# Kernel optimization log

Measured on AMD Instinct MI355X. Metric: run time of the kernel, lower is better.

## Reference

```python
import jax, jax.numpy as jnp
import numpy as np

B, S, D, H, DFF = 2, 2048, 1024, 16, 4096
DK = D // H
EPS = 1e-05


def setup_inputs() -> dict:
    key = jax.random.key(0)
    ks = jax.random.split(key, 10)
    s = 0.02
    return {
        "x": jax.random.normal(ks[0], (B, S, D), jnp.float32),
        "src_mask": jnp.ones((B, 1, 1, S), jnp.int32),
        "wq": jax.random.normal(ks[1], (D, D), jnp.float32) * s,
        "wk": jax.random.normal(ks[2], (D, D), jnp.float32) * s,
        "wv": jax.random.normal(ks[3], (D, D), jnp.float32) * s,
        "wo": jax.random.normal(ks[4], (D, D), jnp.float32) * s,
        "w1": jax.random.normal(ks[5], (D, DFF), jnp.float32) * s,
        "b1": jnp.zeros((DFF,), jnp.float32),
        "w2": jax.random.normal(ks[6], (DFF, D), jnp.float32) * s,
        "b2": jnp.zeros((D,), jnp.float32),
        "gamma1": jnp.ones((), jnp.float32),
        "beta1": jnp.ones((), jnp.float32),
        "gamma2": jnp.ones((), jnp.float32),
        "beta2": jnp.ones((), jnp.float32),
    }


def layer_norm(x, gamma, beta):
    # torch.var uses unbiased estimator (ddof=1); gamma/beta are scalars
    mean = jnp.mean(x, axis=-1, keepdims=True)
    var = jnp.var(x, axis=-1, keepdims=True, ddof=1)
    return (x - mean) * gamma / jnp.sqrt(var + EPS) + beta


def mha(x, wq, wk, wv, wo):
    # Note: source's masked_fill is non-in-place with discarded result -> mask has no effect.
    q = (x @ wq).reshape(B, S, H, DK).transpose(0, 2, 1, 3)
    k = (x @ wk).reshape(B, S, H, DK).transpose(0, 2, 1, 3)
    v = (x @ wv).reshape(B, S, H, DK).transpose(0, 2, 1, 3)
    scores = jnp.einsum('bhqd,bhkd->bhqk', q, k) / jnp.sqrt(jnp.float32(DK))
    attn = jax.nn.softmax(scores, axis=-1)
    out = jnp.einsum('bhqk,bhkd->bhqd', attn, v)
    out = out.transpose(0, 2, 1, 3).reshape(B, S, D)
    return out @ wo


def reference(x, src_mask, wq, wk, wv, wo, w1, b1, w2, b2,
              gamma1, beta1, gamma2, beta2):
    # residual 1: attention (dropout = identity in eval)
    x = layer_norm(x + mha(x, wq, wk, wv, wo), gamma1, beta1)
    # residual 2: FFN
    ff = jax.nn.relu(x @ w1 + b1) @ w2 + b2
    x = layer_norm(x + ff, gamma2, beta2)
    return x
```

## Files before the change

kernel.cpp:

```cpp
#include <hip/hip_runtime.h>
#include <cstdio>

constexpr int B_   = 2;
constexpr int S_   = 2048;
constexpr int D_   = 1024;
constexpr int H_   = 16;
constexpr int DFF_ = 4096;
constexpr int DK_  = D_ / H_;
constexpr int M_   = B_ * S_;
constexpr float EPS_ = 1e-5f;
constexpr size_t MEGE = 1u << 20;
constexpr size_t QKV_STRIDE = 4 * MEGE;
constexpr float QSCALE_ = 0.18033688011112042f;

typedef __attribute__((ext_vector_type(8))) short bf16x8;
typedef __attribute__((ext_vector_type(4))) float f32x4;

__device__ __forceinline__ float bf2f(unsigned int u) {
    return __uint_as_float(u << 16);
}
__device__ __forceinline__ unsigned short f2bf(float f) {
    unsigned int u = __float_as_uint(f);
    unsigned int r = u + 0x7fffu + ((u >> 16) & 1u);
    return (unsigned short)(r >> 16);
// ... 27 lines not shown
        Wt[(size_t)(n0 + ty + p * 8) * K + k0 + tx] = f2bf(t[tx * 33 + ty + p * 8]);
}

__global__ __launch_bounds__(256)
void prep_k(const float* __restrict__ wq, const float* __restrict__ wk,
            const float* __restrict__ wv, const float* __restrict__ wo,
            const float* __restrict__ w1, const float* __restrict__ w2,
            const float* __restrict__ x,
            unsigned short* __restrict__ wqt, unsigned short* __restrict__ wkt,
            unsigned short* __restrict__ wvt, unsigned short* __restrict__ wot,
            unsigned short* __restrict__ w1t, unsigned short* __restrict__ w2t,
            unsigned short* __restrict__ xb)
{
    __shared__ float t[32 * 33];
    const int bid = blockIdx.x;
    if (bid < 4096) {
        const int z = bid >> 10, rem = bid & 1023;
        const float* W = (z == 0) ? wq : (z == 1) ? wk : (z == 2) ? wv : wo;
        unsigned short* Wt = (z == 0) ? wqt : (z == 1) ? wkt : (z == 2) ? wvt : wot;
        tr32(W, Wt, D_, D_, rem & 31, rem >> 5, t);
    } else if (bid < 8192) {
        const int rem = bid - 4096;
        tr32(w1, w1t, D_, DFF_, rem & 127, rem >> 7, t);
    } else if (bid < 12288) {
        const int rem = bid - 8192;
        tr32(w2, w2t, DFF_, D_, rem & 31, rem >> 5, t);
    } else {
        const int i = (bid - 12288) * 256 + threadIdx.x;
        float4 f = reinterpret_cast<const float4*>(x)[i];
        ushort4 u;
        u.x = f2bf(f.x); u.y = f2bf(f.y); u.z = f2bf(f.z); u.w = f2bf(f.w);
        reinterpret_cast<ushort4*>(xb)[i] = u;
    }
}

template<int OMODE, bool RELU>
__global__ __launch_bounds__(1024, 1)
void mg3_k(const unsigned short* __restrict__ A,
           const unsigned short* __restrict__ Bt,
           const float* __restrict__ bias,
           unsigned short* __restrict__ C,
           int M, int N, int K, int Kld)
{
    __shared__ __align__(16) unsigned short As[2][256 * 64];
    __shared__ __align__(16) unsigned short Bs[2][256 * 64];

    const int tid = threadIdx.x;
    const int w = tid >> 6, lane = tid & 63;
    const int l15 = lane & 15, quad = lane >> 4;
    const int wm = w >> 2, wn = w & 3;
    const int m0 = blockIdx.y * 256, n0 = blockIdx.x * 256;
    const int NT = K >> 6;

    const int srow = lane >> 3;
    const int schk = (lane & 7) ^ srow;
    const int rsw  = l15 & 7;

    f32x4 acc[4][4];
    #pragma unroll
    for (int i = 0; i < 4; ++i)
        #pragma unroll
        for (int j = 0; j < 4; ++j) acc[i][j] = (f32x4){0.f, 0.f, 0.f, 0.f};

    auto stageAB = [&](int tile) {
        if (tile >= NT) return;
        const int buf = tile & 1;
// ... 46 lines not shown
        mm16();
        rd(cur, 1);
        __builtin_amdgcn_s_barrier();
        asm volatile("s_waitcnt lgkmcnt(0)" ::: "memory");
        mm16();
    }

    #pragma unroll
    for (int i = 0; i < 4; ++i)
        #pragma unroll
        for (int r = 0; r < 4; ++r) {
            const int m = m0 + wm * 64 + i * 16 + quad * 4 + r;
            #pragma unroll
            for (int j = 0; j < 4; ++j) {
                const int n = n0 + wn * 64 + j * 16 + l15;
                float v = acc[i][j][r];
                if (bias) v += bias[n];
                if (RELU) v = fmaxf(v, 0.0f);
                size_t o;
                if (OMODE == 2) {
                    int mat = n >> 10, nn = n & 1023;
                    int bb = m >> 11, s = m & 2047;
                    int h = nn >> 6, dk = nn & 63;
                    if (mat == 0) v *= QSCALE_;
                    o = (size_t)mat * QKV_STRIDE + (((size_t)bb * H_ + h) * S_ + s) * DK_ + dk;
                } else {
                    o = (size_t)m * N + n;
                }
                C[o] = f2bf(v);
            }
        }
}

template<int BM, int OMODE, bool RELU>
__global__ __launch_bounds__(512, 2)
void mg2_k(const unsigned short* __restrict__ A,
           const unsigned short* __restrict__ Bt,
           const float* __restrict__ bias,
           unsigned short* __restrict__ C,
           int M, int N, int K, int Kld)
{
    constexpr int MI  = BM / 64;
    constexpr int AMH = (BM == 128) ? 2 : 1;
    __shared__ __align__(16) unsigned short As[2][BM * 64];
    __shared__ __align__(16) unsigned short Bs[2][256 * 64];

    const int z = blockIdx.z;
    A  += (size_t)z * K;
    Bt += (size_t)z * K;
    C  += (size_t)z * ((size_t)M * N);

    const int tid  = threadIdx.x;
    const int w    = tid >> 6, lane = tid & 63;
    const int l15  = lane & 15, quad = lane >> 4;
    const int wm   = w >> 2, wn = w & 3;
    const int m0   = blockIdx.y * BM, n0 = blockIdx.x * 256;
    const int NT   = K >> 6;

    const int srow = lane >> 3;
    const int schk = (lane & 7) ^ srow;
    const int rsw  = l15 & 7;

    f32x4 acc[2][MI][2][2];
    #pragma unroll
    for (int mh = 0; mh < 2; ++mh)
        #pragma unroll
        for (int mi = 0; mi < MI; ++mi)
            #pragma unroll
            for (int nh = 0; nh < 2; ++nh)
                #pragma unroll
                for (int nj = 0; nj < 2; ++nj)
                    acc[mh][mi][nh][nj] = (f32x4){0.f, 0.f, 0.f, 0.f};

    bf16x8 aA[AMH][MI][2];
    bf16x8 b0[2][2], b1[2][2];

    auto stage = [&](int tile, int type) {
        if (tile >= NT) return;
        const int buf = tile & 1;
        unsigned short* dst; const unsigned short* src; int r0;
        if (BM == 256) {
            if      (type == 0) { dst = &As[buf][0];        src = A;  r0 = m0; }
            else if (type == 1) { dst = &Bs[buf][0];        src = Bt; r0 = n0; }
            else if (type == 2) { dst = &Bs[buf][128 * 64]; src = Bt; r0 = n0 + 128; }
            else                { dst = &As[buf][128 * 64]; src = A;  r0 = m0 + 128; }
        } else {
            if      (type == 0) { dst = &Bs[buf][0];        src = Bt; r0 = n0; }
            else if (type == 1) { dst = &As[buf][0];        src = A;  r0 = m0; }
            else                { dst = &Bs[buf][128 * 64]; src = Bt; r0 = n0 + 128; }
        }
        const int k0 = tile * 64;
        #pragma unroll
        for (int g = 0; g < 2; ++g) {
            const int r = w * 16 + g * 8 + srow;
            gload_lds16(src + (size_t)(r0 + r) * Kld + k0 + schk * 8,
                        dst + (w * 16 + g * 8) * 64);
        }
    };
    auto rdA = [&](int buf, int mh, int amh) {
        const unsigned short* base = &As[buf][(BM == 256 && mh) ? 128 * 64 : 0];
        #pragma unroll
        for (int mi = 0; mi < MI; ++mi) {
            const int row = (BM == 256) ? (wm * 64 + mi * 16 + l15)
                                        : (wm * 64 + mh * 32 + mi * 16 + l15);
            const unsigned short* rp = base + row * 64;
            aA[amh][mi][0] = *reinterpret_cast<const bf16x8*>(rp + ((quad    ) ^ rsw) * 8);
            aA[amh][mi][1] = *reinterpret_cast<const bf16x8*>(rp + ((quad + 4) ^ rsw) * 8);
        }
    };
    auto rdB = [&](int buf, int nh, bf16x8 (&b)[2][2]) {
        const unsigned short* base = &Bs[buf][nh ? 128 * 64 : 0];
        #pragma unroll
        for (int nj = 0; nj < 2; ++nj) {
            const int row = wn * 32 + nj * 16 + l15;
            const unsigned short* rp = base + row * 64;
            b[nj][0] = *reinterpret_cast<const bf16x8*>(rp + ((quad    ) ^ rsw) * 8);
            b[nj][1] = *reinterpret_cast<const bf16x8*>(rp + ((quad + 4) ^ rsw) * 8);
        }
    };
    auto mm = [&](int mh, int amh, int nh, bf16x8 (&b)[2][2]) {
        __builtin_amdgcn_s_setprio(1);
        #pragma unroll
        for (int mi = 0; mi < MI; ++mi)
            #pragma unroll
            for (int nj = 0; nj < 2; ++nj) {
                acc[mh][mi][nh][nj] = __builtin_amdgcn_mfma_f32_16x16x32_bf16(
                    aA[amh][mi][0], b[nj][0], acc[mh][mi][nh][nj], 0, 0, 0);
                acc[mh][mi][nh][nj] = __builtin_amdgcn_mfma_f32_16x16x32_bf16(
                    aA[amh][mi][1], b[nj][1], acc[mh][mi][nh][nj], 0, 0, 0);
            }
        __builtin_amdgcn_s_setprio(0);
    };

    if (BM == 256) {
        stage(0, 0); stage(0, 1); stage(0, 2); stage(0, 3);
        stage(1, 0); stage(1, 1); stage(1, 2);
    } else {
        stage(0, 0); stage(0, 1); stage(0, 2);
        stage(1, 0); stage(1, 1);
    }

    for (int t = 0; t < NT; ++t) {
        const int cur = t & 1;
        if (t == NT - 1)    asm volatile("s_waitcnt vmcnt(0)" ::: "memory");
        else if (BM == 256) asm volatile("s_waitcnt vmcnt(6)" ::: "memory");
        else                asm volatile("s_waitcnt vmcnt(4)" ::: "memory");
        __builtin_amdgcn_s_barrier();

        if (BM == 256) {
            rdA(cur, 0, 0); rdB(cur, 0, b0); stage(t + 1, 3);
            __builtin_amdgcn_s_barrier();
            asm volatile("s_waitcnt lgkmcnt(0)" ::: "memory");
            mm(0, 0, 0, b0);
            __builtin_amdgcn_s_barrier();
            rdB(cur, 1, b1); stage(t + 2, 0);
            __builtin_amdgcn_s_barrier();
            asm volatile("s_waitcnt lgkmcnt(0)" ::: "memory");
            mm(0, 0, 1, b1);
            __builtin_amdgcn_s_barrier();
            rdA(cur, 1, 0); stage(t + 2, 1);
            __builtin_amdgcn_s_barrier();
            asm volatile("s_waitcnt lgkmcnt(0)" ::: "memory");
            mm(1, 0, 0, b0);
            __builtin_amdgcn_s_barrier();
            stage(t + 2, 2);
            __builtin_amdgcn_s_barrier();
            asm volatile("s_waitcnt lgkmcnt(0)" ::: "memory");
            mm(1, 0, 1, b1);
        } else {
            rdA(cur, 0, 0); rdA(cur, 1, 1); rdB(cur, 0, b0); stage(t + 1, 2);
            __builtin_amdgcn_s_barrier();
            asm volatile("s_waitcnt lgkmcnt(0)" ::: "memory");
            mm(0, 0, 0, b0); mm(1, 1, 0, b0);
            __builtin_amdgcn_s_barrier();
            rdB(cur, 1, b1); stage(t + 2, 0); stage(t + 2, 1);
            __builtin_amdgcn_s_barrier();
            asm volatile("s_waitcnt lgkmcnt(0)" ::: "memory");
            mm(0, 0, 1, b1); mm(1, 1, 1, b1);
        }
    }

    #pragma unroll
    for (int mh = 0; mh < 2; ++mh)
        #pragma unroll
        for (int mi = 0; mi < MI; ++mi) {
            const int mrow = (BM == 256) ? (mh * 128 + wm * 64 + mi * 16)
                                         : (wm * 64 + mh * 32 + mi * 16);
            #pragma unroll
            for (int r = 0; r < 4; ++r) {
                const int m = m0 + mrow + quad * 4 + r;
                #pragma unroll
                for (int nh = 0; nh < 2; ++nh)
                    #pragma unroll
                    for (int nj = 0; nj < 2; ++nj) {
                        const int n = n0 + nh * 128 + wn * 32 + nj * 16 + l15;
                        float v = acc[mh][mi][nh][nj][r];
                        if (bias) v += bias[n];
                        if (RELU) v = fmaxf(v, 0.0f);
                        size_t o;
                        if (OMODE == 2) {
                            int mat = n >> 10, nn = n & 1023;
                            int b = m >> 11, s = m & 2047;
                            int h = nn >> 6, dk = nn & 63;
                            if (mat == 0) v *= QSCALE_;
                            o = (size_t)mat * QKV_STRIDE + (((size_t)b * H_ + h) * S_ + s) * DK_ + dk;
                        } else {
                            o = (size_t)m * N + n;
                        }
                        C[o] = f2bf(v);
                    }
            }
        }
}

__device__ __forceinline__ float wave_sum(float v) {
    #pragma unroll
    for (int off = 32; off > 0; off >>= 1) v += __shfl_down(v, off, 64);
    return v;
}

constexpr int TQ_ = 128;
constexpr int TK_ = 64;
constexpr int NT_ = S_ / TK_;

__global__ __launch_bounds__(512)
void fattn_k(const unsigned short* __restrict__ Qm, const unsigned short* __restrict__ Km,
             const unsigned short* __restrict__ Vm, unsigned short* __restrict__ O)
{
    const int bh  = blockIdx.x >> 4;
    const int qt  = blockIdx.x & 15;
    const int tid = threadIdx.x;
    const int w = tid >> 6, lane = tid & 63;
    const int quad = lane >> 4, l15 = lane & 15;
    const int sw = l15 & 7;

    __shared__ __align__(16) unsigned short Ks[2][TK_][64];
    __shared__ __align__(16) unsigned short Vt[2][80][64];
    __shared__ __align__(16) unsigned short Ps[8][16][64];

    bf16x8 qf0, qf1;
    {
        const unsigned short* qp = Qm + ((size_t)bh * S_ + qt * TQ_ + w * 16 + l15) * DK_;
        qf0 = *reinterpret_cast<const bf16x8*>(qp + quad * 8);
        qf1 = *reinterpret_cast<const bf16x8*>(qp + 32 + quad * 8);
    }

    f32x4 o[4];
    f32x4 o4;
    #pragma unroll
    for (int n = 0; n < 4; ++n) o[n] = (f32x4){0.f, 0.f, 0.f, 0.f};
    o4 = (f32x4){0.f, 0.f, 0.f, 0.f};

    const unsigned short* kg0 = Km + (size_t)bh * S_ * DK_;
    const unsigned short* vg0 = Vm + (size_t)bh * S_ * DK_;
    const int dgrp = tid >> 4;
    const int vkp  = tid & 15;
    const int srow = lane >> 3;
    const int schk = (lane & 7) ^ srow;

    auto stageK = [&](int t, int buf) {
        const unsigned short* src = kg0 + (size_t)t * TK_ * DK_;
        const int wk = w - 4;
        #pragma unroll
        for (int g = 0; g < 2; ++g) {
            const int r0 = wk * 16 + g * 8;
            gload_lds16(src + (size_t)(r0 + srow) * DK_ + schk * 8, &Ks[buf][r0][0]);
        }
    };
    auto loadV = [&](int t, ushort4 (&vp)[4]) {
        const unsigned short* vg = vg0 + (size_t)t * TK_ * DK_;
        #pragma unroll
        for (int p = 0; p < 4; ++p)
            vp[p] = reinterpret_cast<const ushort4*>(vg + (size_t)(vkp + p * 16) * DK_)[dgrp];
    };
    auto storeVt = [&](int buf, ushort4 (&vp)[4]) {
        char* base = reinterpret_cast<char*>(&Vt[buf][dgrp * 4][0]);
        const int cs = vkp >> 1, ch = (vkp & 1) << 3;
        ushort4 pk;
        pk.x = vp[0].x; pk.y = vp[1].x; pk.z = vp[2].x; pk.w = vp[3].x;
        *reinterpret_cast<ushort4*>(base + 0 * 128 + (((cs ^ ((dgrp * 4 + 0) & 7)) << 4) + ch)) = pk;
        pk.x = vp[0].y; pk.y = vp[1].y; pk.z = vp[2].y; pk.w = vp[3].y;
        *reinterpret_cast<ushort4*>(base + 1 * 128 + (((cs ^ ((dgrp * 4 + 1) & 7)) << 4) + ch)) = pk;
        pk.x = vp[0].z; pk.y = vp[1].z; pk.z = vp[2].z; pk.w = vp[3].z;
        *reinterpret_cast<ushort4*>(base + 2 * 128 + (((cs ^ ((dgrp * 4 + 2) & 7)) << 4) + ch)) = pk;
        pk.x = vp[0].w; pk.y = vp[1].w; pk.z = vp[2].w; pk.w = vp[3].w;
        *reinterpret_cast<ushort4*>(base + 3 * 128 + (((cs ^ ((dgrp * 4 + 3) & 7)) << 4) + ch)) = pk;
    };

    if (w >= 4) stageK(0, 0);
    else {
        ushort4 vp0[4];
        loadV(0, vp0);
        storeVt(0, vp0);
    }
    for (int idx = tid; idx < 2 * 16 * 64; idx += 512) {
        const int b  = idx >> 10;
        const int rr = (idx >> 6) & 15;
        const int cc = idx & 63;
        Vt[b][64 + rr][((cc >> 3) ^ (rr & 7)) * 8 + (cc & 7)] =
            (rr == 0) ? (unsigned short)0x3F80 : (unsigned short)0;
    }

    for (int t = 0; t < NT_; ++t) {
        const int cur = t & 1, nxt = cur ^ 1;
        __syncthreads();

        const bool hn = (t + 1 < NT_);
        ushort4 vp[4];
        if (hn) { if (w >= 4) stageK(t + 1, nxt); else loadV(t + 1, vp); }

        f32x4 s[4];
        __builtin_amdgcn_s_setprio(1);
        #pragma unroll
        for (int n = 0; n < 4; ++n) {
            const unsigned short* kp = &Ks[cur][n * 16 + l15][0];
            bf16x8 b0 = *reinterpret_cast<const bf16x8*>(kp + ((quad ^ sw) << 3));
            bf16x8 b1 = *reinterpret_cast<const bf16x8*>(kp + (((quad + 4) ^ sw) << 3));
            f32x4 a2 = (f32x4){0.f, 0.f, 0.f, 0.f};
            a2 = __builtin_amdgcn_mfma_f32_16x16x32_bf16(qf0, b0, a2, 0, 0, 0);
            a2 = __builtin_amdgcn_mfma_f32_16x16x32_bf16(qf1, b1, a2, 0, 0, 0);
            s[n] = a2;
        }
        __builtin_amdgcn_s_setprio(0);

        #pragma unroll
        for (int r = 0; r < 4; ++r) {
            ushort4 pk;
            pk.x = f2bf_rz(exp2_fast(s[0][r]));
            pk.y = f2bf_rz(exp2_fast(s[1][r]));
            pk.z = f2bf_rz(exp2_fast(s[2][r]));
            pk.w = f2bf_rz(exp2_fast(s[3][r]));
            const int R = quad * 4 + r;
            *reinterpret_cast<ushort4*>(
                reinterpret_cast<char*>(&Ps[w][R][0]) +
                ((((l15 >> 1) ^ (R & 7)) << 4) + ((l15 & 1) << 3))) = pk;
        }

        if (hn && w < 4) storeVt(nxt, vp);

        bf16x8 pa0, pa1;
        {
            const unsigned short* pp = &Ps[w][l15][0];
            pa0 = *reinterpret_cast<const bf16x8*>(pp + ((quad ^ sw) << 3));
            pa1 = *reinterpret_cast<const bf16x8*>(pp + (((quad + 4) ^ sw) << 3));
        }
        __builtin_amdgcn_s_setprio(1);
        #pragma unroll
        for (int n = 0; n < 4; ++n) {
            const unsigned short* vb = &Vt[cur][n * 16 + l15][0];
            bf16x8 vb0 = *reinterpret_cast<const bf16x8*>(vb + ((quad ^ sw) << 3));
            bf16x8 vb1 = *reinterpret_cast<const bf16x8*>(vb + (((quad + 4) ^ sw) << 3));
            o[n] = __builtin_amdgcn_mfma_f32_16x16x32_bf16(pa0, vb0, o[n], 0, 0, 0);
            o[n] = __builtin_amdgcn_mfma_f32_16x16x32_bf16(pa1, vb1, o[n], 0, 0, 0);
        }
        {
            const unsigned short* vb = &Vt[cur][64 + l15][0];
            bf16x8 vb40 = *reinterpret_cast<const bf16x8*>(vb + ((quad ^ sw) << 3));
            bf16x8 vb41 = *reinterpret_cast<const bf16x8*>(vb + (((quad + 4) ^ sw) << 3));
            o4 = __builtin_amdgcn_mfma_f32_16x16x32_bf16(pa0, vb40, o4, 0, 0, 0);
            o4 = __builtin_amdgcn_mfma_f32_16x16x32_bf16(pa1, vb41, o4, 0, 0, 0);
        }
        __builtin_amdgcn_s_setprio(0);
    }

    const int b = bh >> 4, h = bh & 15;
    #pragma unroll
    for (int r = 0; r < 4; ++r) {
        float lrv = __shfl(o4[r], lane & 0x30, 64);
        float inv = 1.0f / lrv;
        int q = qt * TQ_ + w * 16 + quad * 4 + r;
        unsigned short* op = O + ((size_t)b * S_ + q) * D_ + h * DK_;
        #pragma unroll
        for (int n = 0; n < 4; ++n)
            op[n * 16 + l15] = f2bf(o[n][r] * inv);
    }
}

template<bool HAS_BIAS, bool RES_F32, bool OUT_F32>
__global__ __launch_bounds__(256)
void lnr_k(const unsigned short* __restrict__ P0, const unsigned short* __restrict__ P1,
           const void* __restrict__ res, const float* __restrict__ bias,
           const float* __restrict__ gp, const float* __restrict__ bp,
           void* __restrict__ Out)
{
    const int row = blockIdx.x;
    const int tid = threadIdx.x;
    const int lane = tid & 63, wave = tid >> 6;
    __shared__ float rs[4], rss[4];

    const size_t i4 = (size_t)row * 256 + tid;
    const ushort4 a = reinterpret_cast<const ushort4*>(P0)[i4];
    const ushort4 b = reinterpret_cast<const ushort4*>(P1)[i4];
    float v0 = bf2f(a.x) + bf2f(b.x);
    float v1 = bf2f(a.y) + bf2f(b.y);
    float v2 = bf2f(a.z) + bf2f(b.z);
    float v3 = bf2f(a.w) + bf2f(b.w);
    if (RES_F32) {
        float4 rv = reinterpret_cast<const float4*>(res)[i4];
        v0 += rv.x; v1 += rv.y; v2 += rv.z; v3 += rv.w;
    } else {
        ushort4 rv = reinterpret_cast<const ushort4*>(res)[i4];
        v0 += bf2f(rv.x); v1 += bf2f(rv.y); v2 += bf2f(rv.z); v3 += bf2f(rv.w);
    }
    if (HAS_BIAS) {
        float4 bv = reinterpret_cast<const float4*>(bias)[tid];
        v0 += bv.x; v1 += bv.y; v2 += bv.z; v3 += bv.w;
    }

// ... 27 lines not shown
                              void* d_out, int out_size, void* d_ws, size_t ws_size,
                              hipStream_t stream)
{
    const float* x   = (const float*)d_in[0];
    const float* wq  = (const float*)d_in[2];
    const float* wk  = (const float*)d_in[3];
    const float* wv  = (const float*)d_in[4];
    const float* wo  = (const float*)d_in[5];
    const float* w1  = (const float*)d_in[6];
    const float* b1  = (const float*)d_in[7];
    const float* w2  = (const float*)d_in[8];
    const float* b2  = (const float*)d_in[9];
    const float* g1  = (const float*)d_in[10];
    const float* be1 = (const float*)d_in[11];
    const float* g2  = (const float*)d_in[12];
    const float* be2 = (const float*)d_in[13];

    unsigned short* ws = (unsigned short*)d_ws;
    const size_t need_bytes = 32 * MEGE * 2;
    if (ws_size < need_bytes) {
        fprintf(stderr, "kernel_launch: ws too small (%zu < %zu)\n", ws_size, need_bytes);
    }
    unsigned short* wqt = ws + 0 * MEGE;
    unsigned short* wkt = ws + 1 * MEGE;
    unsigned short* wvt = ws + 2 * MEGE;
    unsigned short* wot = ws + 3 * MEGE;
    unsigned short* w1t = ws + 4 * MEGE;
    unsigned short* w2t = ws + 8 * MEGE;
    unsigned short* xb  = ws + 12 * MEGE;
    unsigned short* Q   = ws + 16 * MEGE;
    unsigned short* K   = ws + 20 * MEGE;
    unsigned short* V   = ws + 24 * MEGE;
    unsigned short* AO  = ws + 28 * MEGE;
    unsigned short* x1  = xb;
    unsigned short* WP  = ws + 16 * MEGE;
    unsigned short* h1  = ws + 16 * MEGE;
    unsigned short* FP  = ws + 0 * MEGE;

    prep_k<<<dim3(16384), 256, 0, stream>>>(wq, wk, wv, wo, w1, w2, x,
                                            wqt, wkt, wvt, wot, w1t, w2t, xb);

    mg3_k<2, false><<<dim3(3 * D_ / 256, M_ / 256), 1024, 0, stream>>>(
        xb, wqt, nullptr, Q, M_, 3 * D_, D_, D_);

    fattn_k<<<dim3(B_ * H_ * (S_ / TQ_)), 512, 0, stream>>>(Q, K, V, AO);

    mg2_k<128, 0, false><<<dim3(D_ / 256, M_ / 128, 2), 512, 0, stream>>>(
        AO, wot, nullptr, WP, M_, D_, D_ / 2, D_);

    lnr_k<false, true, false><<<dim3(M_), 256, 0, stream>>>(
        WP, WP + 4 * MEGE, x, nullptr, g1, be1, x1);

    mg3_k<0, true><<<dim3(DFF_ / 256, M_ / 256), 1024, 0, stream>>>(
        x1, w1t, b1, h1, M_, DFF_, D_, D_);

    mg2_k<128, 0, false><<<dim3(D_ / 256, M_ / 128, 2), 512, 0, stream>>>(
        h1, w2t, nullptr, FP, M_, D_, DFF_ / 2, DFF_);

    lnr_k<true, false, true><<<dim3(M_), 256, 0, stream>>>(
        FP, FP + 4 * MEGE, x1, b2, g2, be2, d_out);
}
```

Before: 324.7 us.

## Split attention KV range across two blocks and combine partial outputs

The flash-attention kernel now splits the key/value sequence into two halves handled by separate blocks (grid y=2). Each block uses 256 threads, with each wave covering 32 query rows instead of 16 and every wave loading both K and V. Each half writes unnormalized bf16 partial outputs plus its row sums, and a new elementwise combine kernel adds the halves and normalizes. The aim is more parallel blocks and more reuse of each K/V fragment per wave, at the cost of an extra kernel launch, extra global traffic for the partials, and some bf16 rounding of unnormalized sums.

```diff
diff --git a/kernel.cpp b/kernel.cpp
--- a/kernel.cpp
+++ b/kernel.cpp
@@ -382,16 +382,19 @@
     return v;
 }
 
-constexpr int TQ_ = 128;
-constexpr int TK_ = 64;
-constexpr int NT_ = S_ / TK_;
-
-__global__ __launch_bounds__(512)
+constexpr int TQ_  = 128;
+constexpr int TK_  = 64;
+constexpr int NT2_ = (S_ / 2) / TK_;
+
+__global__ __launch_bounds__(256, 3)
 void fattn_k(const unsigned short* __restrict__ Qm, const unsigned short* __restrict__ Km,
-             const unsigned short* __restrict__ Vm, unsigned short* __restrict__ O)
+             const unsigned short* __restrict__ Vm,
+             unsigned short* __restrict__ Po0, unsigned short* __restrict__ Po1,
+             float* __restrict__ Lp)
 {
     const int bh  = blockIdx.x >> 4;
     const int qt  = blockIdx.x & 15;
+    const int kvz = blockIdx.y;
     const int tid = threadIdx.x;
     const int w = tid >> 6, lane = tid & 63;
     const int quad = lane >> 4, l15 = lane & 15;
@@ -399,23 +402,27 @@
 
     __shared__ __align__(16) unsigned short Ks[2][TK_][64];
     __shared__ __align__(16) unsigned short Vt[2][80][64];
-    __shared__ __align__(16) unsigned short Ps[8][16][64];
-
-    bf16x8 qf0, qf1;
-    {
-        const unsigned short* qp = Qm + ((size_t)bh * S_ + qt * TQ_ + w * 16 + l15) * DK_;
-        qf0 = *reinterpret_cast<const bf16x8*>(qp + quad * 8);
-        qf1 = *reinterpret_cast<const bf16x8*>(qp + 32 + quad * 8);
-    }
-
-    f32x4 o[4];
-    f32x4 o4;
-    #pragma unroll
-    for (int n = 0; n < 4; ++n) o[n] = (f32x4){0.f, 0.f, 0.f, 0.f};
-    o4 = (f32x4){0.f, 0.f, 0.f, 0.f};
-
-    const unsigned short* kg0 = Km + (size_t)bh * S_ * DK_;
-    const unsigned short* vg0 = Vm + (size_t)bh * S_ * DK_;
+    __shared__ __align__(16) unsigned short Ps[4][32][64];
+
+    bf16x8 qf[2][2];
+    #pragma unroll
+    for (int i = 0; i < 2; ++i) {
+        const unsigned short* qp = Qm + ((size_t)bh * S_ + qt * TQ_ + w * 32 + i * 16 + l15) * DK_;
+        qf[i][0] = *reinterpret_cast<const bf16x8*>(qp + quad * 8);
+        qf[i][1] = *reinterpret_cast<const bf16x8*>(qp + 32 + quad * 8);
+    }
+
+    f32x4 o[2][4];
+    f32x4 o4[2];
+    #pragma unroll
+    for (int i = 0; i < 2; ++i) {
+        #pragma unroll
+        for (int n = 0; n < 4; ++n) o[i][n] = (f32x4){0.f, 0.f, 0.f, 0.f};
+        o4[i] = (f32x4){0.f, 0.f, 0.f, 0.f};
+    }
+
+    const unsigned short* kg0 = Km + (size_t)bh * S_ * DK_ + (size_t)kvz * (S_ / 2) * DK_;
+    const unsigned short* vg0 = Vm + (size_t)bh * S_ * DK_ + (size_t)kvz * (S_ / 2) * DK_;
     const int dgrp = tid >> 4;
     const int vkp  = tid & 15;
     const int srow = lane >> 3;
@@ -423,10 +430,9 @@
 
     auto stageK = [&](int t, int buf) {
         const unsigned short* src = kg0 + (size_t)t * TK_ * DK_;
-        const int wk = w - 4;
         #pragma unroll
         for (int g = 0; g < 2; ++g) {
-            const int r0 = wk * 16 + g * 8;
+            const int r0 = w * 16 + g * 8;
             gload_lds16(src + (size_t)(r0 + srow) * DK_ + schk * 8, &Ks[buf][r0][0]);
         }
     };
@@ -450,13 +456,13 @@
         *reinterpret_cast<ushort4*>(base + 3 * 128 + (((cs ^ ((dgrp * 4 + 3) & 7)) << 4) + ch)) = pk;
     };
 
-    if (w >= 4) stageK(0, 0);
-    else {
+    stageK(0, 0);
+    {
         ushort4 vp0[4];
         loadV(0, vp0);
         storeVt(0, vp0);
     }
-    for (int idx = tid; idx < 2 * 16 * 64; idx += 512) {
+    for (int idx = tid; idx < 2 * 16 * 64; idx += 256) {
         const int b  = idx >> 10;
         const int rr = (idx >> 6) & 15;
         const int cc = idx & 63;
@@ -464,48 +470,54 @@
             (rr == 0) ? (unsigned short)0x3F80 : (unsigned short)0;
     }
 
-    for (int t = 0; t < NT_; ++t) {
+    for (int t = 0; t < NT2_; ++t) {
         const int cur = t & 1, nxt = cur ^ 1;
         __syncthreads();
 
-        const bool hn = (t + 1 < NT_);
+        const bool hn = (t + 1 < NT2_);
         ushort4 vp[4];
-        if (hn) { if (w >= 4) stageK(t + 1, nxt); else loadV(t + 1, vp); }
-
-        f32x4 s[4];
+        if (hn) { stageK(t + 1, nxt); loadV(t + 1, vp); }
+
+        f32x4 s[2][4];
         __builtin_amdgcn_s_setprio(1);
         #pragma unroll
         for (int n = 0; n < 4; ++n) {
             const unsigned short* kp = &Ks[cur][n * 16 + l15][0];
             bf16x8 b0 = *reinterpret_cast<const bf16x8*>(kp + ((quad ^ sw) << 3));
             bf16x8 b1 = *reinterpret_cast<const bf16x8*>(kp + (((quad + 4) ^ sw) << 3));
-            f32x4 a2 = (f32x4){0.f, 0.f, 0.f, 0.f};
-            a2 = __builtin_amdgcn_mfma_f32_16x16x32_bf16(qf0, b0, a2, 0, 0, 0);
-            a2 = __builtin_amdgcn_mfma_f32_16x16x32_bf16(qf1, b1, a2, 0, 0, 0);
-            s[n] = a2;
+            #pragma unroll
+            for (int i = 0; i < 2; ++i) {
+                f32x4 a2 = (f32x4){0.f, 0.f, 0.f, 0.f};
+                a2 = __builtin_amdgcn_mfma_f32_16x16x32_bf16(qf[i][0], b0, a2, 0, 0, 0);
+                a2 = __builtin_amdgcn_mfma_f32_16x16x32_bf16(qf[i][1], b1, a2, 0, 0, 0);
+                s[i][n] = a2;
+            }
         }
         __builtin_amdgcn_s_setprio(0);
 
         #pragma unroll
-        for (int r = 0; r < 4; ++r) {
-            ushort4 pk;
-            pk.x = f2bf_rz(exp2_fast(s[0][r]));
-            pk.y = f2bf_rz(exp2_fast(s[1][r]));
-            pk.z = f2bf_rz(exp2_fast(s[2][r]));
-            pk.w = f2bf_rz(exp2_fast(s[3][r]));
-            const int R = quad * 4 + r;
-            *reinterpret_cast<ushort4*>(
-                reinterpret_cast<char*>(&Ps[w][R][0]) +
-                ((((l15 >> 1) ^ (R & 7)) << 4) + ((l15 & 1) << 3))) = pk;
-        }
-
-        if (hn && w < 4) storeVt(nxt, vp);
-
-        bf16x8 pa0, pa1;
-        {
-            const unsigned short* pp = &Ps[w][l15][0];
-            pa0 = *reinterpret_cast<const bf16x8*>(pp + ((quad ^ sw) << 3));
-            pa1 = *reinterpret_cast<const bf16x8*>(pp + (((quad + 4) ^ sw) << 3));
+        for (int i = 0; i < 2; ++i)
+            #pragma unroll
+            for (int r = 0; r < 4; ++r) {
+                ushort4 pk;
+                pk.x = f2bf_rz(exp2_fast(s[i][0][r]));
+                pk.y = f2bf_rz(exp2_fast(s[i][1][r]));
+                pk.z = f2bf_rz(exp2_fast(s[i][2][r]));
+                pk.w = f2bf_rz(exp2_fast(s[i][3][r]));
+                const int R = i * 16 + quad * 4 + r;
+                *reinterpret_cast<ushort4*>(
+                    reinterpret_cast<char*>(&Ps[w][R][0]) +
+                    ((((l15 >> 1) ^ (R & 7)) << 4) + ((l15 & 1) << 3))) = pk;
+            }
+
+        if (hn) storeVt(nxt, vp);
+
+        bf16x8 pa[2][2];
+        #pragma unroll
+        for (int i = 0; i < 2; ++i) {
+            const unsigned short* pp = &Ps[w][i * 16 + l15][0];
+            pa[i][0] = *reinterpret_cast<const bf16x8*>(pp + ((quad ^ sw) << 3));
+            pa[i][1] = *reinterpret_cast<const bf16x8*>(pp + (((quad + 4) ^ sw) << 3));
         }
         __builtin_amdgcn_s_setprio(1);
         #pragma unroll
@@ -513,30 +525,58 @@
             const unsigned short* vb = &Vt[cur][n * 16 + l15][0];
             bf16x8 vb0 = *reinterpret_cast<const bf16x8*>(vb + ((quad ^ sw) << 3));
             bf16x8 vb1 = *reinterpret_cast<const bf16x8*>(vb + (((quad + 4) ^ sw) << 3));
-            o[n] = __builtin_amdgcn_mfma_f32_16x16x32_bf16(pa0, vb0, o[n], 0, 0, 0);
-            o[n] = __builtin_amdgcn_mfma_f32_16x16x32_bf16(pa1, vb1, o[n], 0, 0, 0);
+            #pragma unroll
+            for (int i = 0; i < 2; ++i) {
+                o[i][n] = __builtin_amdgcn_mfma_f32_16x16x32_bf16(pa[i][0], vb0, o[i][n], 0, 0, 0);
+                o[i][n] = __builtin_amdgcn_mfma_f32_16x16x32_bf16(pa[i][1], vb1, o[i][n], 0, 0, 0);
+            }
         }
         {
             const unsigned short* vb = &Vt[cur][64 + l15][0];
             bf16x8 vb40 = *reinterpret_cast<const bf16x8*>(vb + ((quad ^ sw) << 3));
             bf16x8 vb41 = *reinterpret_cast<const bf16x8*>(vb + (((quad + 4) ^ sw) << 3));
-            o4 = __builtin_amdgcn_mfma_f32_16x16x32_bf16(pa0, vb40, o4, 0, 0, 0);
-            o4 = __builtin_amdgcn_mfma_f32_16x16x32_bf16(pa1, vb41, o4, 0, 0, 0);
+            #pragma unroll
+            for (int i = 0; i < 2; ++i) {
+                o4[i] = __builtin_amdgcn_mfma_f32_16x16x32_bf16(pa[i][0], vb40, o4[i], 0, 0, 0);
+                o4[i] = __builtin_amdgcn_mfma_f32_16x16x32_bf16(pa[i][1], vb41, o4[i], 0, 0, 0);
+            }
         }
         __builtin_amdgcn_s_setprio(0);
     }
 
+    unsigned short* Po = kvz ? Po1 : Po0;
     const int b = bh >> 4, h = bh & 15;
     #pragma unroll
-    for (int r = 0; r < 4; ++r) {
-        float lrv = __shfl(o4[r], lane & 0x30, 64);
-        float inv = 1.0f / lrv;
-        int q = qt * TQ_ + w * 16 + quad * 4 + r;
-        unsigned short* op = O + ((size_t)b * S_ + q) * D_ + h * DK_;
-        #pragma unroll
-        for (int n = 0; n < 4; ++n)
-            op[n * 16 + l15] = f2bf(o[n][r] * inv);
-    }
+    for (int i = 0; i < 2; ++i)
+        #pragma unroll
+        for (int r = 0; r < 4; ++r) {
+            float lrv = __shfl(o4[i][r], lane & 0x30, 64);
+            int q = qt * TQ_ + w * 32 + i * 16 + quad * 4 + r;
+            if (l15 == 0) Lp[kvz * 65536 + bh * 2048 + q] = lrv;
+            unsigned short* op = Po + ((size_t)b * S_ + q) * D_ + h * DK_;
+            #pragma unroll
+            for (int n = 0; n < 4; ++n)
+                op[n * 16 + l15] = f2bf(o[i][n][r]);
+        }
+}
+
+__global__ __launch_bounds__(256)
+void comb_k(const unsigned short* __restrict__ Po0, const unsigned short* __restrict__ Po1,
+            const float* __restrict__ Lp, unsigned short* __restrict__ AO)
+{
+    const size_t i4 = (size_t)blockIdx.x * 256 + threadIdx.x;
+    const int e = (int)(i4 * 4);
+    const int d = e & 1023, s = (e >> 10) & 2047, b = e >> 21;
+    const int bh = b * 16 + (d >> 6);
+    const float inv = 1.0f / (Lp[bh * 2048 + s] + Lp[65536 + bh * 2048 + s]);
+    const ushort4 a = reinterpret_cast<const ushort4*>(Po0)[i4];
+    const ushort4 c = reinterpret_cast<const ushort4*>(Po1)[i4];
+    ushort4 u;
+    u.x = f2bf((bf2f(a.x) + bf2f(c.x)) * inv);
+    u.y = f2bf((bf2f(a.y) + bf2f(c.y)) * inv);
+    u.z = f2bf((bf2f(a.z) + bf2f(c.z)) * inv);
+    u.w = f2bf((bf2f(a.w) + bf2f(c.w)) * inv);
+    reinterpret_cast<ushort4*>(AO)[i4] = u;
 }
 
 template<bool HAS_BIAS, bool RES_F32, bool OUT_F32>
@@ -630,6 +670,9 @@
     unsigned short* K   = ws + 20 * MEGE;
     unsigned short* V   = ws + 24 * MEGE;
     unsigned short* AO  = ws + 28 * MEGE;
+    unsigned short* Po0 = ws + 12 * MEGE;
+    unsigned short* Po1 = ws + 28 * MEGE;
+    float*          Lp  = (float*)ws;
     unsigned short* x1  = xb;
     unsigned short* WP  = ws + 16 * MEGE;
     unsigned short* h1  = ws + 16 * MEGE;
@@ -641,7 +684,9 @@
     mg3_k<2, false><<<dim3(3 * D_ / 256, M_ / 256), 1024, 0, stream>>>(
         xb, wqt, nullptr, Q, M_, 3 * D_, D_, D_);
 
-    fattn_k<<<dim3(B_ * H_ * (S_ / TQ_)), 512, 0, stream>>>(Q, K, V, AO);
+    fattn_k<<<dim3(B_ * H_ * (S_ / TQ_), 2), 256, 0, stream>>>(Q, K, V, Po0, Po1, Lp);
+
+    comb_k<<<dim3(B_ * S_ * D_ / 1024), 256, 0, stream>>>(Po0, Po1, Lp, AO);
 
     mg2_k<128, 0, false><<<dim3(D_ / 256, M_ / 128, 2), 512, 0, stream>>>(
         AO, wot, nullptr, WP, M_, D_, D_ / 2, D_);
```

After: 348.4 us. +7.3%, slower.

## Pre-transpose V in a separate kernel and accumulate softmax row sums in registers

Applied to the files above, without the earlier changes.

A new kernel transposes V into a [bh][d][s] layout before attention, so the attention kernel can stage V tiles into LDS with async global-to-LDS copies, just as it does for K. This replaces the register-based load and transposed scatter into LDS. The row-sum trick, which used an extra ones-row MFMA, is replaced by accumulating fp32 exp sums in registers and reducing them with shuffles at the end. The cost is an extra kernel launch plus a read and write of V; in exchange the attention inner loop does fewer MFMAs, avoids register staging for V, and sums in fp32 rather than from bf16-rounded probabilities.

```diff
diff --git a/kernel.cpp b/kernel.cpp
--- a/kernel.cpp
+++ b/kernel.cpp
@@ -83,6 +83,25 @@
         u.x = f2bf(f.x); u.y = f2bf(f.y); u.z = f2bf(f.z); u.w = f2bf(f.w);
         reinterpret_cast<ushort4*>(xb)[i] = u;
     }
+}
+
+__global__ __launch_bounds__(256)
+void vtr_k(const unsigned short* __restrict__ V, unsigned short* __restrict__ VT)
+{
+    __shared__ unsigned short t[32][33];
+    const int bh = blockIdx.z;
+    const int s0 = blockIdx.y * 32;
+    const int d0 = blockIdx.x * 32;
+    const int tx = threadIdx.x & 31, ty = threadIdx.x >> 5;
+    const unsigned short* vb = V + (size_t)bh * S_ * DK_;
+    unsigned short* vt = VT + (size_t)bh * DK_ * S_;
+    #pragma unroll
+    for (int p = 0; p < 4; ++p)
+        t[ty + p * 8][tx] = vb[(size_t)(s0 + ty + p * 8) * DK_ + d0 + tx];
+    __syncthreads();
+    #pragma unroll
+    for (int p = 0; p < 4; ++p)
+        vt[(size_t)(d0 + ty + p * 8) * S_ + s0 + tx] = t[tx][ty + p * 8];
 }
 
 template<int OMODE, bool RELU>
@@ -388,7 +407,7 @@
 
 __global__ __launch_bounds__(512)
 void fattn_k(const unsigned short* __restrict__ Qm, const unsigned short* __restrict__ Km,
-             const unsigned short* __restrict__ Vm, unsigned short* __restrict__ O)
+             const unsigned short* __restrict__ VT, unsigned short* __restrict__ O)
 {
     const int bh  = blockIdx.x >> 4;
     const int qt  = blockIdx.x & 15;
@@ -398,7 +417,7 @@
     const int sw = l15 & 7;
 
     __shared__ __align__(16) unsigned short Ks[2][TK_][64];
-    __shared__ __align__(16) unsigned short Vt[2][80][64];
+    __shared__ __align__(16) unsigned short Vs[2][DK_][64];
     __shared__ __align__(16) unsigned short Ps[8][16][64];
 
     bf16x8 qf0, qf1;
@@ -409,15 +428,14 @@
     }
 
     f32x4 o[4];
-    f32x4 o4;
+    float lacc[4];
     #pragma unroll
     for (int n = 0; n < 4; ++n) o[n] = (f32x4){0.f, 0.f, 0.f, 0.f};
-    o4 = (f32x4){0.f, 0.f, 0.f, 0.f};
+    #pragma unroll
+    for (int r = 0; r < 4; ++r) lacc[r] = 0.f;
 
     const unsigned short* kg0 = Km + (size_t)bh * S_ * DK_;
-    const unsigned short* vg0 = Vm + (size_t)bh * S_ * DK_;
-    const int dgrp = tid >> 4;
-    const int vkp  = tid & 15;
+    const unsigned short* vt0 = VT + (size_t)bh * DK_ * S_;
     const int srow = lane >> 3;
     const int schk = (lane & 7) ^ srow;
 
@@ -430,47 +448,23 @@
             gload_lds16(src + (size_t)(r0 + srow) * DK_ + schk * 8, &Ks[buf][r0][0]);
         }
     };
-    auto loadV = [&](int t, ushort4 (&vp)[4]) {
-        const unsigned short* vg = vg0 + (size_t)t * TK_ * DK_;
-        #pragma unroll
-        for (int p = 0; p < 4; ++p)
-            vp[p] = reinterpret_cast<const ushort4*>(vg + (size_t)(vkp + p * 16) * DK_)[dgrp];
-    };
-    auto storeVt = [&](int buf, ushort4 (&vp)[4]) {
-        char* base = reinterpret_cast<char*>(&Vt[buf][dgrp * 4][0]);
-        const int cs = vkp >> 1, ch = (vkp & 1) << 3;
-        ushort4 pk;
-        pk.x = vp[0].x; pk.y = vp[1].x; pk.z = vp[2].x; pk.w = vp[3].x;
-        *reinterpret_cast<ushort4*>(base + 0 * 128 + (((cs ^ ((dgrp * 4 + 0) & 7)) << 4) + ch)) = pk;
-        pk.x = vp[0].y; pk.y = vp[1].y; pk.z = vp[2].y; pk.w = vp[3].y;
-        *reinterpret_cast<ushort4*>(base + 1 * 128 + (((cs ^ ((dgrp * 4 + 1) & 7)) << 4) + ch)) = pk;
-        pk.x = vp[0].z; pk.y = vp[1].z; pk.z = vp[2].z; pk.w = vp[3].z;
-        *reinterpret_cast<ushort4*>(base + 2 * 128 + (((cs ^ ((dgrp * 4 + 2) & 7)) << 4) + ch)) = pk;
-        pk.x = vp[0].w; pk.y = vp[1].w; pk.z = vp[2].w; pk.w = vp[3].w;
-        *reinterpret_cast<ushort4*>(base + 3 * 128 + (((cs ^ ((dgrp * 4 + 3) & 7)) << 4) + ch)) = pk;
-    };
-
-    if (w >= 4) stageK(0, 0);
-    else {
-        ushort4 vp0[4];
-        loadV(0, vp0);
-        storeVt(0, vp0);
-    }
-    for (int idx = tid; idx < 2 * 16 * 64; idx += 512) {
-        const int b  = idx >> 10;
-        const int rr = (idx >> 6) & 15;
-        const int cc = idx & 63;
-        Vt[b][64 + rr][((cc >> 3) ^ (rr & 7)) * 8 + (cc & 7)] =
-            (rr == 0) ? (unsigned short)0x3F80 : (unsigned short)0;
-    }
+    auto stageV = [&](int t, int buf) {
+        const unsigned short* src = vt0 + t * TK_;
+        #pragma unroll
+        for (int g = 0; g < 2; ++g) {
+            const int r0 = w * 16 + g * 8;
+            gload_lds16(src + (size_t)(r0 + srow) * S_ + schk * 8, &Vs[buf][r0][0]);
+        }
+    };
+
+    if (w >= 4) stageK(0, 0); else stageV(0, 0);
 
     for (int t = 0; t < NT_; ++t) {
         const int cur = t & 1, nxt = cur ^ 1;
         __syncthreads();
 
         const bool hn = (t + 1 < NT_);
-        ushort4 vp[4];
-        if (hn) { if (w >= 4) stageK(t + 1, nxt); else loadV(t + 1, vp); }
+        if (hn) { if (w >= 4) stageK(t + 1, nxt); else stageV(t + 1, nxt); }
 
         f32x4 s[4];
         __builtin_amdgcn_s_setprio(1);
@@ -488,18 +482,19 @@
 
         #pragma unroll
         for (int r = 0; r < 4; ++r) {
+            float p0 = exp2_fast(s[0][r]);
+            float p1 = exp2_fast(s[1][r]);
+            float p2 = exp2_fast(s[2][r]);
+            float p3 = exp2_fast(s[3][r]);
+            lacc[r] += (p0 + p1) + (p2 + p3);
             ushort4 pk;
-            pk.x = f2bf_rz(exp2_fast(s[0][r]));
-            pk.y = f2bf_rz(exp2_fast(s[1][r]));
-            pk.z = f2bf_rz(exp2_fast(s[2][r]));
-            pk.w = f2bf_rz(exp2_fast(s[3][r]));
+            pk.x = f2bf_rz(p0); pk.y = f2bf_rz(p1);
+            pk.z = f2bf_rz(p2); pk.w = f2bf_rz(p3);
             const int R = quad * 4 + r;
             *reinterpret_cast<ushort4*>(
                 reinterpret_cast<char*>(&Ps[w][R][0]) +
                 ((((l15 >> 1) ^ (R & 7)) << 4) + ((l15 & 1) << 3))) = pk;
         }
-
-        if (hn && w < 4) storeVt(nxt, vp);
 
         bf16x8 pa0, pa1;
         {
@@ -510,28 +505,30 @@
         __builtin_amdgcn_s_setprio(1);
         #pragma unroll
         for (int n = 0; n < 4; ++n) {
-            const unsigned short* vb = &Vt[cur][n * 16 + l15][0];
+            const unsigned short* vb = &Vs[cur][n * 16 + l15][0];
             bf16x8 vb0 = *reinterpret_cast<const bf16x8*>(vb + ((quad ^ sw) << 3));
             bf16x8 vb1 = *reinterpret_cast<const bf16x8*>(vb + (((quad + 4) ^ sw) << 3));
             o[n] = __builtin_amdgcn_mfma_f32_16x16x32_bf16(pa0, vb0, o[n], 0, 0, 0);
             o[n] = __builtin_amdgcn_mfma_f32_16x16x32_bf16(pa1, vb1, o[n], 0, 0, 0);
         }
-        {
-            const unsigned short* vb = &Vt[cur][64 + l15][0];
-            bf16x8 vb40 = *reinterpret_cast<const bf16x8*>(vb + ((quad ^ sw) << 3));
-            bf16x8 vb41 = *reinterpret_cast<const bf16x8*>(vb + (((quad + 4) ^ sw) << 3));
-            o4 = __builtin_amdgcn_mfma_f32_16x16x32_bf16(pa0, vb40, o4, 0, 0, 0);
-            o4 = __builtin_amdgcn_mfma_f32_16x16x32_bf16(pa1, vb41, o4, 0, 0, 0);
-        }
         __builtin_amdgcn_s_setprio(0);
     }
 
+    #pragma unroll
+    for (int r = 0; r < 4; ++r) {
+        float v = lacc[r];
+        v += __shfl_xor(v, 1, 64);
+        v += __shfl_xor(v, 2, 64);
+        v += __shfl_xor(v, 4, 64);
+        v += __shfl_xor(v, 8, 64);
+        lacc[r] = v;
+    }
+
     const int b = bh >> 4, h = bh & 15;
     #pragma unroll
     for (int r = 0; r < 4; ++r) {
-        float lrv = __shfl(o4[r], lane & 0x30, 64);
-        float inv = 1.0f / lrv;
-        int q = qt * TQ_ + w * 16 + quad * 4 + r;
+        const float inv = 1.0f / lacc[r];
+        const int q = qt * TQ_ + w * 16 + quad * 4 + r;
         unsigned short* op = O + ((size_t)b * S_ + q) * D_ + h * DK_;
         #pragma unroll
         for (int n = 0; n < 4; ++n)
@@ -630,6 +627,7 @@
     unsigned short* K   = ws + 20 * MEGE;
     unsigned short* V   = ws + 24 * MEGE;
     unsigned short* AO  = ws + 28 * MEGE;
+    unsigned short* VTm = ws + 12 * MEGE;
     unsigned short* x1  = xb;
     unsigned short* WP  = ws + 16 * MEGE;
     unsigned short* h1  = ws + 16 * MEGE;
@@ -641,7 +639,9 @@
     mg3_k<2, false><<<dim3(3 * D_ / 256, M_ / 256), 1024, 0, stream>>>(
         xb, wqt, nullptr, Q, M_, 3 * D_, D_, D_);
 
-    fattn_k<<<dim3(B_ * H_ * (S_ / TQ_)), 512, 0, stream>>>(Q, K, V, AO);
+    vtr_k<<<dim3(DK_ / 32, S_ / 32, B_ * H_), 256, 0, stream>>>(V, VTm);
+
+    fattn_k<<<dim3(B_ * H_ * (S_ / TQ_)), 512, 0, stream>>>(Q, K, VTm, AO);
 
     mg2_k<128, 0, false><<<dim3(D_ / 256, M_ / 128, 2), 512, 0, stream>>>(
         AO, wot, nullptr, WP, M_, D_, D_ / 2, D_);
```

Measured after the change: 329.4 us. Within noise of the previous version (+1.5%).

## Replace split-K mg2 GEMM with 16-wave 128x256 tile kernel

Applied to the files above, without the earlier changes.

Replaces the 8-wave templated mg2_k GEMM, used for the output projection and the second FFN matmul, with a 16-wave mg4_k. Each wave now computes a 32x64 sub-tile, and the block keeps the same 128x256 tile and 2-way split-K grid. The staggered multi-stage prefetch schedule is replaced by a simpler double-buffered loop that waits for all loads each iteration. This raises the number of waves available to hide latency and reduces per-wave register use. The cost is less load/compute overlap, since vmcnt(0) is forced every tile, and lower occupancy per CU at one block.

```diff
diff --git a/kernel.cpp b/kernel.cpp
--- a/kernel.cpp
+++ b/kernel.cpp
@@ -195,17 +195,15 @@
         }
 }
 
-template<int BM, int OMODE, bool RELU>
-__global__ __launch_bounds__(512, 2)
-void mg2_k(const unsigned short* __restrict__ A,
+template<bool RELU>
+__global__ __launch_bounds__(1024, 1)
+void mg4_k(const unsigned short* __restrict__ A,
            const unsigned short* __restrict__ Bt,
            const float* __restrict__ bias,
            unsigned short* __restrict__ C,
            int M, int N, int K, int Kld)
 {
-    constexpr int MI  = BM / 64;
-    constexpr int AMH = (BM == 128) ? 2 : 1;
-    __shared__ __align__(16) unsigned short As[2][BM * 64];
+    __shared__ __align__(16) unsigned short As[2][128 * 64];
     __shared__ __align__(16) unsigned short Bs[2][256 * 64];
 
     const int z = blockIdx.z;
@@ -213,165 +211,89 @@
     Bt += (size_t)z * K;
     C  += (size_t)z * ((size_t)M * N);
 
-    const int tid  = threadIdx.x;
-    const int w    = tid >> 6, lane = tid & 63;
-    const int l15  = lane & 15, quad = lane >> 4;
-    const int wm   = w >> 2, wn = w & 3;
-    const int m0   = blockIdx.y * BM, n0 = blockIdx.x * 256;
-    const int NT   = K >> 6;
+    const int tid = threadIdx.x;
+    const int w = tid >> 6, lane = tid & 63;
+    const int l15 = lane & 15, quad = lane >> 4;
+    const int wm = w >> 2, wn = w & 3;
+    const int m0 = blockIdx.y * 128, n0 = blockIdx.x * 256;
+    const int NT = K >> 6;
 
     const int srow = lane >> 3;
     const int schk = (lane & 7) ^ srow;
     const int rsw  = l15 & 7;
 
-    f32x4 acc[2][MI][2][2];
-    #pragma unroll
-    for (int mh = 0; mh < 2; ++mh)
-        #pragma unroll
-        for (int mi = 0; mi < MI; ++mi)
-            #pragma unroll
-            for (int nh = 0; nh < 2; ++nh)
-                #pragma unroll
-                for (int nj = 0; nj < 2; ++nj)
-                    acc[mh][mi][nh][nj] = (f32x4){0.f, 0.f, 0.f, 0.f};
-
-    bf16x8 aA[AMH][MI][2];
-    bf16x8 b0[2][2], b1[2][2];
-
-    auto stage = [&](int tile, int type) {
+    f32x4 acc[2][4];
+    #pragma unroll
+    for (int i = 0; i < 2; ++i)
+        #pragma unroll
+        for (int j = 0; j < 4; ++j) acc[i][j] = (f32x4){0.f, 0.f, 0.f, 0.f};
+
+    auto stageAB = [&](int tile) {
         if (tile >= NT) return;
         const int buf = tile & 1;
-        unsigned short* dst; const unsigned short* src; int r0;
-        if (BM == 256) {
-            if      (type == 0) { dst = &As[buf][0];        src = A;  r0 = m0; }
-            else if (type == 1) { dst = &Bs[buf][0];        src = Bt; r0 = n0; }
-            else if (type == 2) { dst = &Bs[buf][128 * 64]; src = Bt; r0 = n0 + 128; }
-            else                { dst = &As[buf][128 * 64]; src = A;  r0 = m0 + 128; }
-        } else {
-            if      (type == 0) { dst = &Bs[buf][0];        src = Bt; r0 = n0; }
-            else if (type == 1) { dst = &As[buf][0];        src = A;  r0 = m0; }
-            else                { dst = &Bs[buf][128 * 64]; src = Bt; r0 = n0 + 128; }
-        }
         const int k0 = tile * 64;
+        gload_lds16(A + (size_t)(m0 + w * 8 + srow) * Kld + k0 + schk * 8,
+                    &As[buf][w * 8 * 64]);
         #pragma unroll
         for (int g = 0; g < 2; ++g) {
-            const int r = w * 16 + g * 8 + srow;
-            gload_lds16(src + (size_t)(r0 + r) * Kld + k0 + schk * 8,
-                        dst + (w * 16 + g * 8) * 64);
-        }
-    };
-    auto rdA = [&](int buf, int mh, int amh) {
-        const unsigned short* base = &As[buf][(BM == 256 && mh) ? 128 * 64 : 0];
-        #pragma unroll
-        for (int mi = 0; mi < MI; ++mi) {
-            const int row = (BM == 256) ? (wm * 64 + mi * 16 + l15)
-                                        : (wm * 64 + mh * 32 + mi * 16 + l15);
-            const unsigned short* rp = base + row * 64;
-            aA[amh][mi][0] = *reinterpret_cast<const bf16x8*>(rp + ((quad    ) ^ rsw) * 8);
-            aA[amh][mi][1] = *reinterpret_cast<const bf16x8*>(rp + ((quad + 4) ^ rsw) * 8);
-        }
-    };
-    auto rdB = [&](int buf, int nh, bf16x8 (&b)[2][2]) {
-        const unsigned short* base = &Bs[buf][nh ? 128 * 64 : 0];
-        #pragma unroll
-        for (int nj = 0; nj < 2; ++nj) {
-            const int row = wn * 32 + nj * 16 + l15;
-            const unsigned short* rp = base + row * 64;
-            b[nj][0] = *reinterpret_cast<const bf16x8*>(rp + ((quad    ) ^ rsw) * 8);
-            b[nj][1] = *reinterpret_cast<const bf16x8*>(rp + ((quad + 4) ^ rsw) * 8);
-        }
-    };
-    auto mm = [&](int mh, int amh, int nh, bf16x8 (&b)[2][2]) {
+            const int r = w * 16 + g * 8;
+            gload_lds16(Bt + (size_t)(n0 + r + srow) * Kld + k0 + schk * 8,
+                        &Bs[buf][r * 64]);
+        }
+    };
+
+    bf16x8 a[2], b[4];
+    auto rd = [&](int buf, int h) {
+        #pragma unroll
+        for (int i = 0; i < 2; ++i) {
+            const unsigned short* rp = &As[buf][(wm * 32 + i * 16 + l15) * 64];
+            a[i] = *reinterpret_cast<const bf16x8*>(rp + (((quad + 4 * h) ^ rsw) << 3));
+        }
+        #pragma unroll
+        for (int j = 0; j < 4; ++j) {
+            const unsigned short* rp = &Bs[buf][(wn * 64 + j * 16 + l15) * 64];
+            b[j] = *reinterpret_cast<const bf16x8*>(rp + (((quad + 4 * h) ^ rsw) << 3));
+        }
+    };
+    auto mm8 = [&]() {
         __builtin_amdgcn_s_setprio(1);
         #pragma unroll
-        for (int mi = 0; mi < MI; ++mi)
+        for (int i = 0; i < 2; ++i)
             #pragma unroll
-            for (int nj = 0; nj < 2; ++nj) {
-                acc[mh][mi][nh][nj] = __builtin_amdgcn_mfma_f32_16x16x32_bf16(
-                    aA[amh][mi][0], b[nj][0], acc[mh][mi][nh][nj], 0, 0, 0);
-                acc[mh][mi][nh][nj] = __builtin_amdgcn_mfma_f32_16x16x32_bf16(
-                    aA[amh][mi][1], b[nj][1], acc[mh][mi][nh][nj], 0, 0, 0);
-            }
+            for (int j = 0; j < 4; ++j)
+                acc[i][j] = __builtin_amdgcn_mfma_f32_16x16x32_bf16(a[i], b[j], acc[i][j], 0, 0, 0);
         __builtin_amdgcn_s_setprio(0);
     };
 
-    if (BM == 256) {
-        stage(0, 0); stage(0, 1); stage(0, 2); stage(0, 3);
-        stage(1, 0); stage(1, 1); stage(1, 2);
-    } else {
-        stage(0, 0); stage(0, 1); stage(0, 2);
-        stage(1, 0); stage(1, 1);
-    }
+    stageAB(0);
 
     for (int t = 0; t < NT; ++t) {
         const int cur = t & 1;
-        if (t == NT - 1)    asm volatile("s_waitcnt vmcnt(0)" ::: "memory");
-        else if (BM == 256) asm volatile("s_waitcnt vmcnt(6)" ::: "memory");
-        else                asm volatile("s_waitcnt vmcnt(4)" ::: "memory");
+        asm volatile("s_waitcnt vmcnt(0)" ::: "memory");
         __builtin_amdgcn_s_barrier();
-
-        if (BM == 256) {
-            rdA(cur, 0, 0); rdB(cur, 0, b0); stage(t + 1, 3);
-            __builtin_amdgcn_s_barrier();
-            asm volatile("s_waitcnt lgkmcnt(0)" ::: "memory");
-            mm(0, 0, 0, b0);
-            __builtin_amdgcn_s_barrier();
-            rdB(cur, 1, b1); stage(t + 2, 0);
-            __builtin_amdgcn_s_barrier();
-            asm volatile("s_waitcnt lgkmcnt(0)" ::: "memory");
-            mm(0, 0, 1, b1);
-            __builtin_amdgcn_s_barrier();
-            rdA(cur, 1, 0); stage(t + 2, 1);
-            __builtin_amdgcn_s_barrier();
-            asm volatile("s_waitcnt lgkmcnt(0)" ::: "memory");
-            mm(1, 0, 0, b0);
-            __builtin_amdgcn_s_barrier();
-            stage(t + 2, 2);
-            __builtin_amdgcn_s_barrier();
-            asm volatile("s_waitcnt lgkmcnt(0)" ::: "memory");
-            mm(1, 0, 1, b1);
-        } else {
-            rdA(cur, 0, 0); rdA(cur, 1, 1); rdB(cur, 0, b0); stage(t + 1, 2);
-            __builtin_amdgcn_s_barrier();
-            asm volatile("s_waitcnt lgkmcnt(0)" ::: "memory");
-            mm(0, 0, 0, b0); mm(1, 1, 0, b0);
-            __builtin_amdgcn_s_barrier();
-            rdB(cur, 1, b1); stage(t + 2, 0); stage(t + 2, 1);
-            __builtin_amdgcn_s_barrier();
-            asm volatile("s_waitcnt lgkmcnt(0)" ::: "memory");
-            mm(0, 0, 1, b1); mm(1, 1, 1, b1);
-        }
-    }
-
-    #pragma unroll
-    for (int mh = 0; mh < 2; ++mh)
-        #pragma unroll
-        for (int mi = 0; mi < MI; ++mi) {
-            const int mrow = (BM == 256) ? (mh * 128 + wm * 64 + mi * 16)
-                                         : (wm * 64 + mh * 32 + mi * 16);
+        stageAB(t + 1);
+        rd(cur, 0);
+        __builtin_amdgcn_s_barrier();
+        asm volatile("s_waitcnt lgkmcnt(0)" ::: "memory");
+        mm8();
+        rd(cur, 1);
+        __builtin_amdgcn_s_barrier();
+        asm volatile("s_waitcnt lgkmcnt(0)" ::: "memory");
+        mm8();
+    }
+
+    #pragma unroll
+    for (int i = 0; i < 2; ++i)
+        #pragma unroll
+        for (int r = 0; r < 4; ++r) {
+            const int m = m0 + wm * 32 + i * 16 + quad * 4 + r;
             #pragma unroll
-            for (int r = 0; r < 4; ++r) {
-                const int m = m0 + mrow + quad * 4 + r;
-                #pragma unroll
-                for (int nh = 0; nh < 2; ++nh)
-                    #pragma unroll
-                    for (int nj = 0; nj < 2; ++nj) {
-                        const int n = n0 + nh * 128 + wn * 32 + nj * 16 + l15;
-                        float v = acc[mh][mi][nh][nj][r];
-                        if (bias) v += bias[n];
-                        if (RELU) v = fmaxf(v, 0.0f);
-                        size_t o;
-                        if (OMODE == 2) {
-                            int mat = n >> 10, nn = n & 1023;
-                            int b = m >> 11, s = m & 2047;
-                            int h = nn >> 6, dk = nn & 63;
-                            if (mat == 0) v *= QSCALE_;
-                            o = (size_t)mat * QKV_STRIDE + (((size_t)b * H_ + h) * S_ + s) * DK_ + dk;
-                        } else {
-                            o = (size_t)m * N + n;
-                        }
-                        C[o] = f2bf(v);
-                    }
+            for (int j = 0; j < 4; ++j) {
+                const int n = n0 + wn * 64 + j * 16 + l15;
+                float v = acc[i][j][r];
+                if (bias) v += bias[n];
+                if (RELU) v = fmaxf(v, 0.0f);
+                C[(size_t)m * N + n] = f2bf(v);
             }
         }
 }
@@ -643,7 +565,7 @@
 
     fattn_k<<<dim3(B_ * H_ * (S_ / TQ_)), 512, 0, stream>>>(Q, K, V, AO);
 
-    mg2_k<128, 0, false><<<dim3(D_ / 256, M_ / 128, 2), 512, 0, stream>>>(
+    mg4_k<false><<<dim3(D_ / 256, M_ / 128, 2), 1024, 0, stream>>>(
         AO, wot, nullptr, WP, M_, D_, D_ / 2, D_);
 
     lnr_k<false, true, false><<<dim3(M_), 256, 0, stream>>>(
@@ -652,7 +574,7 @@
     mg3_k<0, true><<<dim3(DFF_ / 256, M_ / 256), 1024, 0, stream>>>(
         x1, w1t, b1, h1, M_, DFF_, D_, D_);
 
-    mg2_k<128, 0, false><<<dim3(D_ / 256, M_ / 128, 2), 512, 0, stream>>>(
+    mg4_k<false><<<dim3(D_ / 256, M_ / 128, 2), 1024, 0, stream>>>(
         h1, w2t, nullptr, FP, M_, D_, DFF_ / 2, DFF_);
 
     lnr_k<true, false, true><<<dim3(M_), 256, 0, stream>>>(
```

Measured after the change: 344.5 us. 6.1% more time.
